# Optimization experiments

Hardware: AMD Instinct MI355X
Metric: run time of the kernel (lower is better)

The kernel has to match this reference:

```python
import jax, jax.numpy as jnp
import numpy as np

BATCH = 4096
IN_F = 1024
OUT_F = 1024
GRID_SIZE = 8
SPLINE_ORDER = 3
SCALE_SPLINE = 1.0


def setup_inputs() -> dict:
    key = jax.random.key(0)
    kx, kb, ks = jax.random.split(key, 3)
    # inputs live on the spline domain [-1, 1]
    x = jax.random.uniform(kx, (BATCH, IN_F), jnp.float32, -1.0, 1.0)
    # kaiming_uniform_(a=sqrt(5)) on (out,in) -> U(-1/sqrt(in), 1/sqrt(in))
    bound = 1.0 / float(np.sqrt(IN_F))
    base_weight = jax.random.uniform(kb, (OUT_F, IN_F), jnp.float32, -bound, bound)
    # normal(mean=0, std=0.1), (out, in, grid_size + spline_order)
    spline_weight = 0.1 * jax.random.normal(ks, (OUT_F, IN_F, GRID_SIZE + SPLINE_ORDER), jnp.float32)
    # uniform knot vector with spacing h = 2/grid_size over [-1,1], extended by
    # spline_order knots on each side so Cox-de Boor yields grid_size+spline_order bases
    h = 2.0 / GRID_SIZE
    grid = jnp.arange(-SPLINE_ORDER, GRID_SIZE + SPLINE_ORDER + 1, dtype=jnp.float32) * h - 1.0
    return {"x": x, "base_weight": base_weight, "spline_weight": spline_weight, "grid": grid}


def b_spline_basis(x, grid, k):
    # x: (batch, in), grid: (grid_size + 2k + 1,) shared across (out, in) pairs
    xe = x[..., None]  # (b, i, 1)
    # degree-0: indicator of knot interval -> (b, i, grid_size + 2k)
    basis = ((xe >= grid[:-1]) & (xe < grid[1:])).astype(x.dtype)
    for d in range(1, k + 1):  # Cox-de Boor recursion up to degree k
        left_denom = grid[d:-1] - grid[:-(d + 1)]
        right_denom = grid[d + 1:] - grid[1:-d]
        left_denom = jnp.where(left_denom > 0, left_denom, 1.0)
        right_denom = jnp.where(right_denom > 0, right_denom, 1.0)
        basis = ((xe - grid[:-(d + 1)]) / left_denom * basis[..., :-1]
                 + (grid[d + 1:] - xe) / right_denom * basis[..., 1:])
    return basis  # (b, i, grid_size + k)


def reference(x, base_weight, spline_weight, grid):
    base_output = x @ base_weight.T  # (b, out)
    basis = b_spline_basis(x, grid, SPLINE_ORDER)  # (b, i, L), L = grid_size + k
    # grid is identical for every (out, in) pair, so the per-(o,i) basis of the
    # original collapses to a per-i basis; einsum 'bil,oil->bo' is the same math.
    spline_output = jnp.einsum('bil,oil->bo', basis, spline_weight)
    return base_output + SCALE_SPLINE * spline_output
```

## Files before the change

kernel.cpp:

```cpp
#include <hip/hip_runtime.h>
#include <hip/hip_bf16.h>
#include <cstdint>

#define BATCH 4096
#define INF   1024
#define OUTF  1024
#define LCH   12
#define KTOT  (INF*LCH)

#define BM 128
#define BN 128
#define IC 8
#define BK (IC*LCH)
#define NCHUNK (INF/IC)
#define LDA 96
#define THREADS 512

typedef __bf16 bf16x8 __attribute__((ext_vector_type(8)));
typedef float  f32x4  __attribute__((ext_vector_type(4)));
typedef unsigned long long ull;

struct alignas(16) U2 { ull x, y; };

__device__ __forceinline__ unsigned short f2bf(float f) {
  unsigned int u = __builtin_bit_cast(unsigned int, f);
  u += 0x7FFFu + ((u >> 16) & 1u);
  return (unsigned short)(u >> 16);
}

__device__ __forceinline__ void async_copy16(const void* g, void* l) {
  __builtin_amdgcn_global_load_lds(
      (const __attribute__((address_space(1))) unsigned int*)g,
      (__attribute__((address_space(3))) unsigned int*)l,
      16, 0, 0);
}

#define PIPE_BARRIER() do {                                        \
  asm volatile("s_waitcnt vmcnt(4) lgkmcnt(0)" ::: "memory");      \
  __builtin_amdgcn_sched_barrier(0);                               \
  __builtin_amdgcn_s_barrier();                                    \
  __builtin_amdgcn_sched_barrier(0);                               \
} while (0)

__global__ __launch_bounds__(256) void kan_build_wt(
    const float* __restrict__ sw,
    const float* __restrict__ bw,
    unsigned short* __restrict__ Wt)
{
  int idx = blockIdx.x * 256 + threadIdx.x;
  int o = idx >> 10;
  int i = idx & 1023;
  const float* s = sw + (size_t)(o * 1024 + i) * 11;
  unsigned short v[12];
#pragma unroll
  for (int l = 0; l < 11; ++l) v[l] = f2bf(s[l]);
  v[11] = f2bf(bw[o * 1024 + i]);
  unsigned short* d = Wt + (size_t)o * KTOT + i * 12;
  *reinterpret_cast<ushort4*>(d + 0) = make_ushort4(v[0], v[1], v[2],  v[3]);
  *reinterpret_cast<ushort4*>(d + 4) = make_ushort4(v[4], v[5], v[6],  v[7]);
  *reinterpret_cast<ushort4*>(d + 8) = make_ushort4(v[8], v[9], v[10], v[11]);
}

__global__ __launch_bounds__(THREADS, 1) void kan_gemm(
    const float* __restrict__ x,
    const unsigned short* __restrict__ Wt,
    float* __restrict__ out)
{
  __shared__ unsigned short Abuf[2][BM * LDA];
  __shared__ unsigned short Bbuf[3][(BK / 8) * BN * 8];

  const int tid  = threadIdx.x;
  const int lane = tid & 63;
  const int wid  = tid >> 6;
  const int wm   = (wid >> 1) * 32;
  const int wn   = (wid & 1) * 64;
  const int bm   = (int)blockIdx.x >> 3;
  const int bn   = (int)blockIdx.x & 7;
  const int lr   = lane & 15;
  const int lk   = lane >> 4;

  const int ab  = tid >> 2;
  const int ai0 = (tid & 3) * 2;
  const float* xrow = x + (size_t)(bm * BM + ab) * INF + ai0;

  unsigned short* Acur = Abuf[0]; unsigned short* Aalt = Abuf[1];
  unsigned short* Bcur = Bbuf[0]; unsigned short* Bnxt = Bbuf[1];
  unsigned short* Bnn  = Bbuf[2];

  f32x4 acc[2][4] = {};

  auto stageB = [&](int c, unsigned short* Bd) {
#pragma unroll
    for (int q = 0; q < 3; ++q) {
      int g  = (wid * 3 + q) * 64 + lane;
      int kk = g >> 7;
      int oo = g & 127;
      const unsigned short* src = Wt + (size_t)(bn * BN + oo) * KTOT + (c * BK + kk * 8);
      async_copy16(src, Bd + (wid * 3 + q) * 512);
    }
  };

  auto buildA = [&](float2 xv, unsigned short* Ad) {
    ull W[6];
#pragma unroll
    for (int j = 0; j < 2; ++j) {
      float xx = (j == 0) ? xv.x : xv.y;
      float u  = fmaf(xx, 4.0f, 7.0f);
      float fm = floorf(u);
      int   mi = (int)fm;
      float t  = u - fm;
      float s  = 1.0f - t;
      float t2 = t * t, t3 = t2 * t;
      float w0 = (s * s * s) * (1.0f / 6.0f);
      float w3 = t3 * (1.0f / 6.0f);
      float w1 = fmaf(0.5f, t3, 2.0f / 3.0f) - t2;
      float w2 = 1.0f - w0 - w1 - w3;
      int ls = mi - 3;

      ull W64 = (ull)f2bf(w0)
              | ((ull)f2bf(w1) << 16)
              | ((ull)f2bf(w2) << 32)
              | ((ull)f2bf(w3) << 48);
      int sh = ls << 4;
      int a  = sh & 63;
      ull lo = W64 << a;
      ull hi = a ? (W64 >> (64 - a)) : 0ull;
      W[3 * j + 0] = (sh < 64) ? lo : 0ull;
      W[3 * j + 1] = (sh < 64) ? hi : lo;
      W[3 * j + 2] = ((sh < 64) ? 0ull : hi) | ((ull)f2bf(xx) << 48);
    }
    U2* p = reinterpret_cast<U2*>(&Ad[ab * LDA + ai0 * 12]);
    U2 u0; u0.x = W[0]; u0.y = W[1];
    U2 u1; u1.x = W[2]; u1.y = W[3];
    U2 u2; u2.x = W[4]; u2.y = W[5];
    p[0] = u0; p[1] = u1; p[2] = u2;
  };

  float2 x0 = *reinterpret_cast<const float2*>(xrow);
  stageB(0, Bcur);
  buildA(x0, Acur);
  float2 xa = *reinterpret_cast<const float2*>(xrow + IC);
  stageB(1, Bnxt);
  PIPE_BARRIER();

  for (int c = 0; c < NCHUNK; ++c) {
    int cf = (c + 2 < NCHUNK) ? (c + 2) : (NCHUNK - 1);
    float2 xb = *reinterpret_cast<const float2*>(xrow + cf * IC);
    stageB(cf, Bnn);
    buildA(xa, Aalt);

#pragma unroll
    for (int kk32 = 0; kk32 < 3; ++kk32) {
      bf16x8 af[2], bfr[4];
#pragma unroll
      for (int mf = 0; mf < 2; ++mf)
        af[mf] = *reinterpret_cast<const bf16x8*>(
            &Acur[(wm + mf * 16 + lr) * LDA + kk32 * 32 + lk * 8]);
#pragma unroll
      for (int nf = 0; nf < 4; ++nf)
        bfr[nf] = *reinterpret_cast<const bf16x8*>(
            &Bcur[(((kk32 * 4 + lk) * 128) + (wn + nf * 16 + lr)) * 8]);
#pragma unroll
      for (int mf = 0; mf < 2; ++mf)
#pragma unroll
        for (int nf = 0; nf < 4; ++nf)
          acc[mf][nf] = __builtin_amdgcn_mfma_f32_16x16x32_bf16(
              af[mf], bfr[nf], acc[mf][nf], 0, 0, 0);
    }

    PIPE_BARRIER();

    unsigned short* t = Bcur; Bcur = Bnxt; Bnxt = Bnn; Bnn = t;
    t = Acur; Acur = Aalt; Aalt = t;
    xa = xb;
  }

#pragma unroll
  for (int mf = 0; mf < 2; ++mf) {
#pragma unroll
    for (int v = 0; v < 4; ++v) {
      int row = bm * BM + wm + mf * 16 + lk * 4 + v;
      float* orow = out + (size_t)row * OUTF + bn * BN + wn + lr;
#pragma unroll
      for (int nf = 0; nf < 4; ++nf)
        orow[nf * 16] = acc[mf][nf][v];
    }
  }
}

extern "C" void kernel_launch(void* const* d_in, const int* in_sizes, int n_in,
                              void* d_out, int out_size, void* d_ws, size_t ws_size,
                              hipStream_t stream) {
  const float* x  = (const float*)d_in[0];
  const float* bw = (const float*)d_in[1];
  const float* sw = (const float*)d_in[2];
  float* out = (float*)d_out;

  unsigned short* Wt = (unsigned short*)d_ws;
  if (ws_size < (size_t)OUTF * KTOT * sizeof(unsigned short)) return;

  kan_build_wt<<<(OUTF * INF) / 256, 256, 0, stream>>>(sw, bw, Wt);
  kan_gemm<<<(BATCH / BM) * (OUTF / BN), THREADS, 0, stream>>>(x, Wt, out);
}
```

Measured before the change: 166.0 us.

## Switch to 32x32x16 MFMA with split-K warp groups and LDS reduction

Replaces the 16x16x32 MFMA tiling with 32x32x16 MFMAs. The eight waves are split into two groups that each handle half of the K chunk, and each wave covers a 64x64 output quadrant. The A tile is rearranged into the same k-granule-major layout as B, and the two groups' partial sums are combined through LDS in a reduction epilogue before the store. The aim is fewer LDS fragment loads per MFMA and higher MFMA throughput, at the cost of an extra LDS reduction pass and one group of waves sitting idle during the final store.

```diff
diff --git a/kernel.cpp b/kernel.cpp
--- a/kernel.cpp
+++ b/kernel.cpp
@@ -13,11 +13,12 @@
 #define IC 8
 #define BK (IC*LCH)
 #define NCHUNK (INF/IC)
-#define LDA 96
+#define NGRAN 12
 #define THREADS 512
+#define BUFSZ (NGRAN*128*8)
 
 typedef __bf16 bf16x8 __attribute__((ext_vector_type(8)));
-typedef float  f32x4  __attribute__((ext_vector_type(4)));
+typedef float  f32x16 __attribute__((ext_vector_type(16)));
 typedef unsigned long long ull;
 
 struct alignas(16) U2 { ull x, y; };
@@ -66,37 +67,40 @@
     const unsigned short* __restrict__ Wt,
     float* __restrict__ out)
 {
-  __shared__ unsigned short Abuf[2][BM * LDA];
-  __shared__ unsigned short Bbuf[3][(BK / 8) * BN * 8];
+  __shared__ alignas(16) unsigned short smem[5 * BUFSZ];
 
   const int tid  = threadIdx.x;
   const int lane = tid & 63;
   const int wid  = tid >> 6;
-  const int wm   = (wid >> 1) * 32;
-  const int wn   = (wid & 1) * 64;
+  const int g    = wid >> 2;
+  const int q    = wid & 3;
+  const int qm   = q >> 1;
+  const int qn   = q & 1;
+  const int lo   = lane & 31;
+  const int lh   = lane >> 5;
   const int bm   = (int)blockIdx.x >> 3;
   const int bn   = (int)blockIdx.x & 7;
-  const int lr   = lane & 15;
-  const int lk   = lane >> 4;
-
-  const int ab  = tid >> 2;
-  const int ai0 = (tid & 3) * 2;
+
+  const int ab  = tid & 127;
+  const int ai0 = (tid >> 7) << 1;
   const float* xrow = x + (size_t)(bm * BM + ab) * INF + ai0;
 
-  unsigned short* Acur = Abuf[0]; unsigned short* Aalt = Abuf[1];
-  unsigned short* Bcur = Bbuf[0]; unsigned short* Bnxt = Bbuf[1];
-  unsigned short* Bnn  = Bbuf[2];
-
-  f32x4 acc[2][4] = {};
+  unsigned short* Bcur = smem;
+  unsigned short* Bnxt = smem + BUFSZ;
+  unsigned short* Bnn  = smem + 2 * BUFSZ;
+  unsigned short* Acur = smem + 3 * BUFSZ;
+  unsigned short* Aalt = smem + 4 * BUFSZ;
+
+  f32x16 acc[2][2] = {};
 
   auto stageB = [&](int c, unsigned short* Bd) {
 #pragma unroll
-    for (int q = 0; q < 3; ++q) {
-      int g  = (wid * 3 + q) * 64 + lane;
-      int kk = g >> 7;
-      int oo = g & 127;
+    for (int qq = 0; qq < 3; ++qq) {
+      int G  = (wid * 3 + qq) * 64 + lane;
+      int kk = G >> 7;
+      int oo = G & 127;
       const unsigned short* src = Wt + (size_t)(bn * BN + oo) * KTOT + (c * BK + kk * 8);
-      async_copy16(src, Bd + (wid * 3 + q) * 512);
+      async_copy16(src, Bd + (wid * 3 + qq) * 512);
     }
   };
 
@@ -123,25 +127,30 @@
               | ((ull)f2bf(w3) << 48);
       int sh = ls << 4;
       int a  = sh & 63;
-      ull lo = W64 << a;
-      ull hi = a ? (W64 >> (64 - a)) : 0ull;
-      W[3 * j + 0] = (sh < 64) ? lo : 0ull;
-      W[3 * j + 1] = (sh < 64) ? hi : lo;
-      W[3 * j + 2] = ((sh < 64) ? 0ull : hi) | ((ull)f2bf(xx) << 48);
-    }
-    U2* p = reinterpret_cast<U2*>(&Ad[ab * LDA + ai0 * 12]);
+      ull lop = W64 << a;
+      ull hip_ = a ? (W64 >> (64 - a)) : 0ull;
+      W[3 * j + 0] = (sh < 64) ? lop : 0ull;
+      W[3 * j + 1] = (sh < 64) ? hip_ : lop;
+      W[3 * j + 2] = ((sh < 64) ? 0ull : hip_) | ((ull)f2bf(xx) << 48);
+    }
+    U2* p = reinterpret_cast<U2*>(Ad);
+    const int g0 = (ai0 >> 1) * 3;
     U2 u0; u0.x = W[0]; u0.y = W[1];
     U2 u1; u1.x = W[2]; u1.y = W[3];
     U2 u2; u2.x = W[4]; u2.y = W[5];
-    p[0] = u0; p[1] = u1; p[2] = u2;
+    p[(g0 + 0) * 128 + ab] = u0;
+    p[(g0 + 1) * 128 + ab] = u1;
+    p[(g0 + 2) * 128 + ab] = u2;
   };
 
-  float2 x0 = *reinterpret_cast<const float2*>(xrow);
+  float2 x0v = *reinterpret_cast<const float2*>(xrow);
   stageB(0, Bcur);
-  buildA(x0, Acur);
+  buildA(x0v, Acur);
   float2 xa = *reinterpret_cast<const float2*>(xrow + IC);
   stageB(1, Bnxt);
   PIPE_BARRIER();
+
+  const int g3 = g * 3;
 
   for (int c = 0; c < NCHUNK; ++c) {
     int cf = (c + 2 < NCHUNK) ? (c + 2) : (NCHUNK - 1);
@@ -150,22 +159,16 @@
     buildA(xa, Aalt);
 
 #pragma unroll
-    for (int kk32 = 0; kk32 < 3; ++kk32) {
-      bf16x8 af[2], bfr[4];
-#pragma unroll
-      for (int mf = 0; mf < 2; ++mf)
-        af[mf] = *reinterpret_cast<const bf16x8*>(
-            &Acur[(wm + mf * 16 + lr) * LDA + kk32 * 32 + lk * 8]);
-#pragma unroll
-      for (int nf = 0; nf < 4; ++nf)
-        bfr[nf] = *reinterpret_cast<const bf16x8*>(
-            &Bcur[(((kk32 * 4 + lk) * 128) + (wn + nf * 16 + lr)) * 8]);
-#pragma unroll
-      for (int mf = 0; mf < 2; ++mf)
-#pragma unroll
-        for (int nf = 0; nf < 4; ++nf)
-          acc[mf][nf] = __builtin_amdgcn_mfma_f32_16x16x32_bf16(
-              af[mf], bfr[nf], acc[mf][nf], 0, 0, 0);
+    for (int s = 0; s < 3; ++s) {
+      const int kk = (g3 + s) * 2 + lh;
+      bf16x8 af0 = *reinterpret_cast<const bf16x8*>(&Acur[(kk * 128 + qm * 64 + lo) * 8]);
+      bf16x8 af1 = *reinterpret_cast<const bf16x8*>(&Acur[(kk * 128 + qm * 64 + 32 + lo) * 8]);
+      bf16x8 bf0 = *reinterpret_cast<const bf16x8*>(&Bcur[(kk * 128 + qn * 64 + lo) * 8]);
+      bf16x8 bf1 = *reinterpret_cast<const bf16x8*>(&Bcur[(kk * 128 + qn * 64 + 32 + lo) * 8]);
+      acc[0][0] = __builtin_amdgcn_mfma_f32_32x32x16_bf16(af0, bf0, acc[0][0], 0, 0, 0);
+      acc[0][1] = __builtin_amdgcn_mfma_f32_32x32x16_bf16(af0, bf1, acc[0][1], 0, 0, 0);
+      acc[1][0] = __builtin_amdgcn_mfma_f32_32x32x16_bf16(af1, bf0, acc[1][0], 0, 0, 0);
+      acc[1][1] = __builtin_amdgcn_mfma_f32_32x32x16_bf16(af1, bf1, acc[1][1], 0, 0, 0);
     }
 
     PIPE_BARRIER();
@@ -175,15 +178,33 @@
     xa = xb;
   }
 
-#pragma unroll
-  for (int mf = 0; mf < 2; ++mf) {
-#pragma unroll
-    for (int v = 0; v < 4; ++v) {
-      int row = bm * BM + wm + mf * 16 + lk * 4 + v;
-      float* orow = out + (size_t)row * OUTF + bn * BN + wn + lr;
-#pragma unroll
-      for (int nf = 0; nf < 4; ++nf)
-        orow[nf * 16] = acc[mf][nf][v];
+  asm volatile("s_waitcnt vmcnt(0) lgkmcnt(0)" ::: "memory");
+  __builtin_amdgcn_s_barrier();
+
+  float* M = reinterpret_cast<float*>(smem);
+  if (g == 1) {
+#pragma unroll
+    for (int mf = 0; mf < 2; ++mf)
+#pragma unroll
+      for (int nf = 0; nf < 2; ++nf)
+#pragma unroll
+        for (int r = 0; r < 16; ++r)
+          M[(((q * 4 + mf * 2 + nf) * 16 + r) << 6) + lane] = acc[mf][nf][r];
+  }
+  __syncthreads();
+  if (g == 0) {
+#pragma unroll
+    for (int mf = 0; mf < 2; ++mf) {
+#pragma unroll
+      for (int nf = 0; nf < 2; ++nf) {
+#pragma unroll
+        for (int r = 0; r < 16; ++r) {
+          float v = acc[mf][nf][r] + M[(((q * 4 + mf * 2 + nf) * 16 + r) << 6) + lane];
+          int row = bm * BM + qm * 64 + mf * 32 + (r & 3) + 8 * (r >> 2) + 4 * lh;
+          int col = bn * BN + qn * 64 + nf * 32 + lo;
+          out[(size_t)row * OUTF + col] = v;
+        }
+      }
     }
   }
 }
```

Result: slower. 203.9 us (+22.8%).
